# Performance work log

Hardware: AMD Instinct MI355X
Metric: run time of the kernel (lower is better)

## Reference

```python
import jax, jax.numpy as jnp
import numpy as np

N = 50000       # nodes
E = 1600000     # edges (avg degree 32)
IN = 64         # in_channels
ED = 16         # edge_dim
H = 128         # hidden_channels


def setup_inputs() -> dict:
    key = jax.random.key(0)
    ks = jax.random.split(key, 32)
    rn = lambda k, shape, s: jax.random.normal(k, shape, jnp.float32) * s
    inp = {}
    inp['x'] = rn(ks[0], (N, IN), 1.0)
    inp['edge_index'] = jax.random.randint(ks[1], (2, E), 0, N, dtype=jnp.int64)
    inp['edge_attr'] = rn(ks[2], (E, ED), 1.0)
    # per-layer params: edge linear (ED -> node_dim), MLP (d_in->H, H->H)
    node_dims = [IN, H, H]
    i = 3
    for l, d in enumerate(node_dims):
        inp[f'We{l}'] = rn(ks[i], (ED, d), 1.0 / np.sqrt(ED)); i += 1
        inp[f'be{l}'] = jnp.zeros((d,), jnp.float32)
        inp[f'W1_{l}'] = rn(ks[i], (d, H), 1.0 / np.sqrt(d)); i += 1
        inp[f'b1_{l}'] = jnp.zeros((H,), jnp.float32)
        inp[f'W2_{l}'] = rn(ks[i], (H, H), 1.0 / np.sqrt(H)); i += 1
        inp[f'b2_{l}'] = jnp.zeros((H,), jnp.float32)
    inp['Wlin'] = rn(ks[i], (H, 1), 1.0 / np.sqrt(H))
    inp['blin'] = jnp.zeros((1,), jnp.float32)
    return inp


def gine_conv(x, src, dst, ea, We, be, W1, b1, W2, b2):
    # message: relu(x_j + Lin_e(edge_attr)); aggregate: sum into dst; eps=0
    msg = jax.nn.relu(x[src] + ea @ We + be)            # [E, d]
    agg = jax.ops.segment_sum(msg, dst, num_segments=x.shape[0])  # [N, d]
    h = x + agg                                          # (1+eps)*x + agg, eps=0
    return jax.nn.relu(h @ W1 + b1) @ W2 + b2            # MLP


def reference(x, edge_index, edge_attr,
              We0, be0, W1_0, b1_0, W2_0, b2_0,
              We1, be1, W1_1, b1_1, W2_1, b2_1,
              We2, be2, W1_2, b1_2, W2_2, b2_2,
              Wlin, blin):
    src, dst = edge_index[0], edge_index[1]
    h = jax.nn.relu(gine_conv(x, src, dst, edge_attr, We0, be0, W1_0, b1_0, W2_0, b2_0))
    h = jax.nn.relu(gine_conv(h, src, dst, edge_attr, We1, be1, W1_1, b1_1, W2_1, b2_1))
    h = jax.nn.relu(gine_conv(h, src, dst, edge_attr, We2, be2, W1_2, b1_2, W2_2, b2_2))
    out = jax.nn.sigmoid(h @ Wlin + blin)                # [N, 1]
    return out.squeeze(-1)                               # [N]
```

## Files before the change

### kernel.cpp

```cpp
#include <hip/hip_runtime.h>
#include <math.h>


#define BLK 256

typedef __attribute__((ext_vector_type(2))) float f32x2;
typedef __attribute__((ext_vector_type(16))) float f32x16;

__device__ inline f32x2 pk_fma(f32x2 a, f32x2 b, f32x2 c) {
    f32x2 d;
    asm("v_pk_fma_f32 %0, %1, %2, %3" : "=v"(d) : "v"(a), "v"(b), "v"(c));
    return d;
}
__device__ inline f32x2 pk_fma_s(f32x2 a, f32x2 b, f32x2 c) {
    f32x2 d;
    asm("v_pk_fma_f32 %0, %1, %2, %3" : "=v"(d) : "s"(a), "v"(b), "v"(c));
    return d;
}
__device__ inline f32x16 sload16(const float* p) {
    f32x16 r;
    asm volatile("s_load_dwordx16 %0, %1, 0x0" : "=s"(r) : "s"(p));
    return r;
}


__global__ void detect_kernel(const unsigned int* __restrict__ ei, int* __restrict__ flag) {
    int t = blockIdx.x * blockDim.x + threadIdx.x;
    if (t < 1024) {
        if (ei[2 * t + 1] != 0u) atomicOr(flag, 1);
    }
}

__global__ void convert_hist_kernel(const int* __restrict__ ei32, const long long* __restrict__ ei64,
                                    const int* __restrict__ flag, int E,
                                    unsigned int* __restrict__ drank,
                                    int* __restrict__ counts) {
    int e = blockIdx.x * blockDim.x + threadIdx.x;
    if (e >= E) return;
    int d;
    if (*flag) d = ei32[E + e];
    else       d = (int)ei64[E + e];
    unsigned int r = (unsigned int)atomicAdd(&counts[d], 1);
    drank[e] = (unsigned int)d | (r << 16);
}

__global__ void scan_kernel(const int* __restrict__ counts, int* __restrict__ offsets, int n) {
    __shared__ int tsum[256];
    __shared__ int texcl[256];
    int t = threadIdx.x;
    int chunk = (n + 255) >> 8;
    int b = t * chunk, e = min(b + chunk, n);
    int s = 0;
    for (int i = b; i < e; i++) s += counts[i];
    tsum[t] = s;
    __syncthreads();
    if (t == 0) {
        int run = 0;
        for (int i = 0; i < 256; i++) { texcl[i] = run; run += tsum[i]; }
        offsets[n] = run;
    }
    __syncthreads();
    int run = texcl[t];
    for (int i = b; i < e; i++) { offsets[i] = run; run += counts[i]; }
}

__global__ void scatter_perm_kernel(const unsigned int* __restrict__ drank,
                                    const int* __restrict__ offsets,
                                    int* __restrict__ perm, int E) {
    int e = blockIdx.x * blockDim.x + threadIdx.x;
    if (e >= E) return;
    unsigned int v = drank[e];
    perm[offsets[v & 0xffffu] + (int)(v >> 16)] = e;
}

__global__ __launch_bounds__(256) void gather_ea_kernel(
    const int* __restrict__ perm,
    const int* __restrict__ ei32, const long long* __restrict__ ei64,
    const int* __restrict__ flag,
    const float4* __restrict__ ea4,
    int* __restrict__ srcp, float4* __restrict__ eap4, int E) {
    int t = blockIdx.x * blockDim.x + threadIdx.x;
    int p = t >> 2, q = t & 3;
    if (p >= E) return;
    int e = perm[p];
    if (q == 0) {
        int s;
        if (*flag) s = ei32[e];
        else       s = (int)ei64[e];
        srcp[p] = s;
    }
    eap4[(size_t)p * 4 + q] = ea4[(size_t)e * 4 + q];
}


__global__ __launch_bounds__(256) void aggregate64s_kernel(
    const float* __restrict__ x, const float* __restrict__ eap,
    const int* __restrict__ srcp,
    const float* __restrict__ We, const float* __restrict__ be,
    const int* __restrict__ offsets,
    float* __restrict__ h, int n) {
    constexpr int D = 64;
    int lane = threadIdx.x & 63;
    int node = __builtin_amdgcn_readfirstlane(blockIdx.x * 4 + (threadIdx.x >> 6));
    if (node >= n) return;
    int c0 = lane;

    f32x2 wp[8];
#pragma unroll
    for (int t = 0; t < 8; t++) {
        f32x2 v; v.x = We[(2 * t) * D + c0]; v.y = We[(2 * t + 1) * D + c0];
        wp[t] = v;
    }
    float bias = be[c0];
    float acc  = x[(size_t)node * D + c0];
    int p  = __builtin_amdgcn_readfirstlane(offsets[node]);
    int pe = __builtin_amdgcn_readfirstlane(offsets[node + 1]);

    for (; p + 4 <= pe; p += 4) {
        f32x16 r0 = sload16(eap + (size_t)p * 16);
        f32x16 r1 = sload16(eap + (size_t)(p + 1) * 16);
        f32x16 r2 = sload16(eap + (size_t)(p + 2) * 16);
        f32x16 r3 = sload16(eap + (size_t)(p + 3) * 16);
        int s0 = srcp[p], s1 = srcp[p + 1], s2 = srcp[p + 2], s3 = srcp[p + 3];
        float xv0 = x[(size_t)s0 * D + c0];
        float xv1 = x[(size_t)s1 * D + c0];
        float xv2 = x[(size_t)s2 * D + c0];
        float xv3 = x[(size_t)s3 * D + c0];
        asm volatile("s_waitcnt lgkmcnt(0)" : "+s"(r0), "+s"(r1), "+s"(r2), "+s"(r3));
#define EDGE_S(RU, XV)                                          \
        {                                                       \
            f32x2 prod; prod.x = (XV) + bias; prod.y = 0.f;     \
            _Pragma("unroll")                                   \
            for (int t = 0; t < 8; t++) {                       \
                f32x2 e; e.x = RU[2 * t]; e.y = RU[2 * t + 1];  \
                prod = pk_fma_s(e, wp[t], prod);                \
            }                                                   \
            acc += fmaxf(prod.x + prod.y, 0.f);                 \
        }
        EDGE_S(r0, xv0)
        EDGE_S(r1, xv1)
        EDGE_S(r2, xv2)
        EDGE_S(r3, xv3)
#undef EDGE_S
    }
    for (; p < pe; p++) {
        int s = srcp[p];
        float xv0 = x[(size_t)s * D + c0];
        const float4* er = (const float4*)(eap + (size_t)p * 16);
        float4 e0 = er[0], e1 = er[1], e2 = er[2], e3 = er[3];
        f32x2 ev[8];
        ev[0].x = e0.x; ev[0].y = e0.y;  ev[1].x = e0.z; ev[1].y = e0.w;
        ev[2].x = e1.x; ev[2].y = e1.y;  ev[3].x = e1.z; ev[3].y = e1.w;
        ev[4].x = e2.x; ev[4].y = e2.y;  ev[5].x = e2.z; ev[5].y = e2.w;
        ev[6].x = e3.x; ev[6].y = e3.y;  ev[7].x = e3.z; ev[7].y = e3.w;
        f32x2 prod; prod.x = xv0 + bias; prod.y = 0.f;
#pragma unroll
        for (int t = 0; t < 8; t++) prod = pk_fma(ev[t], wp[t], prod);
        acc += fmaxf(prod.x + prod.y, 0.f);
    }
    h[(size_t)node * D + c0] = acc;
}

__global__ __launch_bounds__(256) void aggregate128s_kernel(
    const float* __restrict__ x, const float* __restrict__ eap,
    const int* __restrict__ srcp,
    const float* __restrict__ We, const float* __restrict__ be,
    const int* __restrict__ offsets,
    float* __restrict__ h, int n) {
    constexpr int D = 128;
    int lane = threadIdx.x & 63;
    int node = __builtin_amdgcn_readfirstlane(blockIdx.x * 4 + (threadIdx.x >> 6));
    if (node >= n) return;
    int c0 = lane * 2;

    f32x2 wp[2][8];
#pragma unroll
    for (int j = 0; j < 2; j++)
#pragma unroll
        for (int t = 0; t < 8; t++) {
            f32x2 v; v.x = We[(2 * t) * D + c0 + j]; v.y = We[(2 * t + 1) * D + c0 + j];
            wp[j][t] = v;
        }
    float bias[2], acc[2];
#pragma unroll
    for (int j = 0; j < 2; j++) {
        bias[j] = be[c0 + j];
        acc[j]  = x[(size_t)node * D + c0 + j];
    }
    int p  = __builtin_amdgcn_readfirstlane(offsets[node]);
    int pe = __builtin_amdgcn_readfirstlane(offsets[node + 1]);

    for (; p + 4 <= pe; p += 4) {
        f32x16 r0 = sload16(eap + (size_t)p * 16);
        f32x16 r1 = sload16(eap + (size_t)(p + 1) * 16);
        f32x16 r2 = sload16(eap + (size_t)(p + 2) * 16);
        f32x16 r3 = sload16(eap + (size_t)(p + 3) * 16);
        int s0 = srcp[p], s1 = srcp[p + 1], s2 = srcp[p + 2], s3 = srcp[p + 3];
        float2 xv0 = *(const float2*)(x + (size_t)s0 * D + c0);
        float2 xv1 = *(const float2*)(x + (size_t)s1 * D + c0);
        float2 xv2 = *(const float2*)(x + (size_t)s2 * D + c0);
        float2 xv3 = *(const float2*)(x + (size_t)s3 * D + c0);
        asm volatile("s_waitcnt lgkmcnt(0)" : "+s"(r0), "+s"(r1), "+s"(r2), "+s"(r3));
#define EDGE_S2(RU, XV)                                             \
        {                                                           \
            f32x2 p0; p0.x = (XV).x + bias[0]; p0.y = 0.f;          \
            f32x2 p1; p1.x = (XV).y + bias[1]; p1.y = 0.f;          \
            _Pragma("unroll")                                       \
            for (int t = 0; t < 8; t++) {                           \
                f32x2 e; e.x = RU[2 * t]; e.y = RU[2 * t + 1];      \
                p0 = pk_fma_s(e, wp[0][t], p0);                     \
                p1 = pk_fma_s(e, wp[1][t], p1);                     \
            }                                                       \
            acc[0] += fmaxf(p0.x + p0.y, 0.f);                      \
            acc[1] += fmaxf(p1.x + p1.y, 0.f);                      \
        }
        EDGE_S2(r0, xv0)
        EDGE_S2(r1, xv1)
        EDGE_S2(r2, xv2)
        EDGE_S2(r3, xv3)
#undef EDGE_S2
    }
    for (; p < pe; p++) {
        int s = srcp[p];
        float2 xv = *(const float2*)(x + (size_t)s * D + c0);
        const float4* er = (const float4*)(eap + (size_t)p * 16);
        float4 e0 = er[0], e1 = er[1], e2 = er[2], e3 = er[3];
        f32x2 ev[8];
        ev[0].x = e0.x; ev[0].y = e0.y;  ev[1].x = e0.z; ev[1].y = e0.w;
        ev[2].x = e1.x; ev[2].y = e1.y;  ev[3].x = e1.z; ev[3].y = e1.w;
        ev[4].x = e2.x; ev[4].y = e2.y;  ev[5].x = e2.z; ev[5].y = e2.w;
        ev[6].x = e3.x; ev[6].y = e3.y;  ev[7].x = e3.z; ev[7].y = e3.w;
        f32x2 p0; p0.x = xv.x + bias[0]; p0.y = 0.f;
        f32x2 p1; p1.x = xv.y + bias[1]; p1.y = 0.f;
#pragma unroll
        for (int t = 0; t < 8; t++) {
            p0 = pk_fma(ev[t], wp[0][t], p0);
            p1 = pk_fma(ev[t], wp[1][t], p1);
        }
        acc[0] += fmaxf(p0.x + p0.y, 0.f);
        acc[1] += fmaxf(p1.x + p1.y, 0.f);
    }
    *(float2*)(h + (size_t)node * D + c0) = make_float2(acc[0], acc[1]);
}

template <int K>
__global__ __launch_bounds__(256) void gemm_kernel(
    const float* __restrict__ A, const float* __restrict__ B,
    const float* __restrict__ bias, float* __restrict__ C, int n) {
    __shared__ __align__(16) float As[16][36];
    __shared__ __align__(16) float Bs[16][128];
    int t = threadIdx.x;
    int row0 = blockIdx.x * 32;
    int tr = t >> 5, tc = t & 31;
    float acc[4][4];
#pragma unroll
    for (int r = 0; r < 4; r++)
#pragma unroll
        for (int c = 0; c < 4; c++) acc[r][c] = 0.f;

    int lr = t & 31, lk = (t >> 5) * 2;
    int bk = t >> 4, bc = (t & 15) * 8;

    int grow = row0 + lr;
    const float* aptr = A + (size_t)grow * K + lk;
    float2 a;
    if (grow < n) a = *(const float2*)aptr;
    else a = make_float2(0.f, 0.f);
    const float4* bp = (const float4*)(B + (size_t)bk * 128 + bc);
    float4 b0 = bp[0], b1 = bp[1];

#pragma unroll 1
    for (int ks = 0; ks < K; ks += 16) {
        As[lk + 0][lr] = a.x; As[lk + 1][lr] = a.y;
        *(float4*)&Bs[bk][bc] = b0;
        *(float4*)&Bs[bk][bc + 4] = b1;
        __syncthreads();
        if (ks + 16 < K) {
            if (grow < n) a = *(const float2*)(aptr + ks + 16);
            const float4* bp2 = (const float4*)(B + (size_t)(ks + 16 + bk) * 128 + bc);
            b0 = bp2[0]; b1 = bp2[1];
        }
#pragma unroll
        for (int kk = 0; kk < 16; kk++) {
            float4 a0 = *(const float4*)&As[kk][tr * 4];
            float4 bv = *(const float4*)&Bs[kk][tc * 4];
            float ar[4] = {a0.x, a0.y, a0.z, a0.w};
            float bc4[4] = {bv.x, bv.y, bv.z, bv.w};
#pragma unroll
            for (int r = 0; r < 4; r++)
#pragma unroll
                for (int c = 0; c < 4; c++) acc[r][c] = fmaf(ar[r], bc4[c], acc[r][c]);
        }
        __syncthreads();
    }
    float4 bb = *(const float4*)(bias + tc * 4);
#pragma unroll
    for (int r = 0; r < 4; r++) {
        int gr = row0 + tr * 4 + r;
        if (gr < n) {
            float4 v;
            v.x = fmaxf(acc[r][0] + bb.x, 0.f);
            v.y = fmaxf(acc[r][1] + bb.y, 0.f);
            v.z = fmaxf(acc[r][2] + bb.z, 0.f);
            v.w = fmaxf(acc[r][3] + bb.w, 0.f);
            *(float4*)(C + (size_t)gr * 128 + tc * 4) = v;
        }
    }
}

__global__ __launch_bounds__(256) void final_kernel(
    const float* __restrict__ x, const float* __restrict__ Wlin,
    const float* __restrict__ blin, float* __restrict__ out, int n) {
    int lane = threadIdx.x & 63;
    int node = blockIdx.x * 4 + (threadIdx.x >> 6);
    if (node >= n) return;
    float2 w = *(const float2*)(Wlin + lane * 2);
    float2 xv = *(const float2*)(x + (size_t)node * 128 + lane * 2);
    float v = xv.x * w.x + xv.y * w.y;
#pragma unroll
    for (int off = 32; off; off >>= 1) v += __shfl_down(v, off, 64);
    if (lane == 0) out[node] = 1.f / (1.f + expf(-(v + blin[0])));
}

extern "C" void kernel_launch(void* const* d_in, const int* in_sizes, int n_in,
                              void* d_out, int out_size, void* d_ws, size_t ws_size,
                              hipStream_t stream) {
    const float* x_in = (const float*)d_in[0];
    const void* ei    = d_in[1];
    const float* ea   = (const float*)d_in[2];
    const float* We[3]  = {(const float*)d_in[3], (const float*)d_in[9],  (const float*)d_in[15]};
    const float* be[3]  = {(const float*)d_in[4], (const float*)d_in[10], (const float*)d_in[16]};
    const float* W1[3]  = {(const float*)d_in[5], (const float*)d_in[11], (const float*)d_in[17]};
    const float* b1[3]  = {(const float*)d_in[6], (const float*)d_in[12], (const float*)d_in[18]};
    const float* W2[3]  = {(const float*)d_in[7], (const float*)d_in[13], (const float*)d_in[19]};
    const float* b2[3]  = {(const float*)d_in[8], (const float*)d_in[14], (const float*)d_in[20]};
    const float* Wlin = (const float*)d_in[21];
    const float* blin = (const float*)d_in[22];
    float* out = (float*)d_out;

    const int N = in_sizes[0] / 64;
    const int E = in_sizes[1] / 2;

    size_t off = 0;
    auto alloc = [&](size_t bytes) {
        void* p = (char*)d_ws + off;
        off += (bytes + 255) & ~(size_t)255;
        return p;
    };
    int*          flag    = (int*)alloc(4);
    unsigned int* drank   = (unsigned int*)alloc((size_t)E * 4);
    int*          counts  = (int*)alloc((size_t)N * 4);
    int*          offsets = (int*)alloc((size_t)(N + 1) * 4);
    int*          perm    = (int*)alloc((size_t)E * 4);
    int*          srcp    = (int*)alloc((size_t)E * 4);
    float*        eap     = (float*)alloc((size_t)E * 16 * 4);
    float*        bufA    = (float*)alloc((size_t)N * 128 * 4);
    float*        bufB    = (float*)alloc((size_t)N * 128 * 4);
    float*        bufC    = (float*)alloc((size_t)N * 128 * 4);

    hipMemsetAsync(flag, 0, 4, stream);
    hipMemsetAsync(counts, 0, (size_t)N * 4, stream);

    int egrid = (E + BLK - 1) / BLK;
    detect_kernel<<<4, BLK, 0, stream>>>((const unsigned int*)ei, flag);
    convert_hist_kernel<<<egrid, BLK, 0, stream>>>((const int*)ei, (const long long*)ei, flag, E,
                                                   drank, counts);
    scan_kernel<<<1, BLK, 0, stream>>>(counts, offsets, N);
    scatter_perm_kernel<<<egrid, BLK, 0, stream>>>(drank, offsets, perm, E);
    int g4grid = ((E * 4) + BLK - 1) / BLK;
    gather_ea_kernel<<<g4grid, BLK, 0, stream>>>(perm, (const int*)ei, (const long long*)ei, flag,
                                                 (const float4*)ea, srcp, (float4*)eap, E);

    int ngrid4 = (N + 3) / 4;
    int ggrid  = (N + 31) / 32;

    aggregate64s_kernel<<<ngrid4, BLK, 0, stream>>>(x_in, eap, srcp, We[0], be[0], offsets, bufA, N);
    gemm_kernel<64><<<ggrid, BLK, 0, stream>>>(bufA, W1[0], b1[0], bufB, N);
    gemm_kernel<128><<<ggrid, BLK, 0, stream>>>(bufB, W2[0], b2[0], bufC, N);
    aggregate128s_kernel<<<ngrid4, BLK, 0, stream>>>(bufC, eap, srcp, We[1], be[1], offsets, bufA, N);
    gemm_kernel<128><<<ggrid, BLK, 0, stream>>>(bufA, W1[1], b1[1], bufB, N);
    gemm_kernel<128><<<ggrid, BLK, 0, stream>>>(bufB, W2[1], b2[1], bufC, N);
    aggregate128s_kernel<<<ngrid4, BLK, 0, stream>>>(bufC, eap, srcp, We[2], be[2], offsets, bufA, N);
    gemm_kernel<128><<<ggrid, BLK, 0, stream>>>(bufA, W1[2], b1[2], bufB, N);
    gemm_kernel<128><<<ggrid, BLK, 0, stream>>>(bufB, W2[2], b2[2], bufC, N);

    final_kernel<<<ngrid4, BLK, 0, stream>>>(bufC, Wlin, blin, out, N);
}
```

Measured before the change: 938.5 us.

## Replace FP32 SIMT GEMMs with split-bf16 MFMA GEMMs using pre-split weights

Swaps the shared-memory FP32 FMA GEMM for a wave-level MFMA GEMM. Activations are split on the fly into bf16 hi/lo parts, and the weights are split once per call by a new conversion kernel into transposed hi/lo bf16 arrays. Each product uses three bf16 MFMAs (hi*hi, hi*lo, lo*hi) to stay close to FP32 accuracy while using the matrix cores. The cost is an extra small kernel launch, no LDS reuse of B (read from global/L2 per wave), and slightly reduced precision from dropping the lo*lo term.

Result: slower. 976.6 us (+4.1%).

```diff
diff --git a/kernel.cpp b/kernel.cpp
--- a/kernel.cpp
+++ b/kernel.cpp
@@ -6,6 +6,8 @@
 
 typedef __attribute__((ext_vector_type(2))) float f32x2;
 typedef __attribute__((ext_vector_type(16))) float f32x16;
+typedef __attribute__((ext_vector_type(8))) short bf16x8;
+typedef __attribute__((ext_vector_type(4))) float f32x4;
 
 __device__ inline f32x2 pk_fma(f32x2 a, f32x2 b, f32x2 c) {
     f32x2 d;
@@ -90,6 +92,32 @@
         srcp[p] = s;
     }
     eap4[(size_t)p * 4 + q] = ea4[(size_t)e * 4 + q];
+}
+
+struct WConvArgs {
+    const float* src[6];
+    short* hi[6];
+    short* lo[6];
+    int K[6];
+};
+
+__global__ void wconv_kernel(WConvArgs a) {
+    int b = blockIdx.x;
+    int m, base;
+    if (b < 32) { m = 0; base = 0; }
+    else { m = 1 + (b - 32) / 64; base = 32 + (m - 1) * 64; }
+    int idx = (b - base) * 256 + threadIdx.x;
+    int K = a.K[m];
+    if (idx >= K * 128) return;
+    int k = idx >> 7, nn = idx & 127;
+    float w = a.src[m][idx];
+    unsigned bits = __float_as_uint(w);
+    short hi = (short)(bits >> 16);
+    float hif = __uint_as_float(bits & 0xffff0000u);
+    float r = w - hif;
+    short lo = (short)(__float_as_uint(r) >> 16);
+    a.hi[m][(size_t)nn * K + k] = hi;
+    a.lo[m][(size_t)nn * K + k] = lo;
 }
 
 
@@ -244,66 +272,56 @@
 }
 
 template <int K>
-__global__ __launch_bounds__(256) void gemm_kernel(
-    const float* __restrict__ A, const float* __restrict__ B,
-    const float* __restrict__ bias, float* __restrict__ C, int n) {
-    __shared__ __align__(16) float As[16][36];
-    __shared__ __align__(16) float Bs[16][128];
-    int t = threadIdx.x;
-    int row0 = blockIdx.x * 32;
-    int tr = t >> 5, tc = t & 31;
-    float acc[4][4];
-#pragma unroll
-    for (int r = 0; r < 4; r++)
-#pragma unroll
-        for (int c = 0; c < 4; c++) acc[r][c] = 0.f;
-
-    int lr = t & 31, lk = (t >> 5) * 2;
-    int bk = t >> 4, bc = (t & 15) * 8;
-
-    int grow = row0 + lr;
-    const float* aptr = A + (size_t)grow * K + lk;
-    float2 a;
-    if (grow < n) a = *(const float2*)aptr;
-    else a = make_float2(0.f, 0.f);
-    const float4* bp = (const float4*)(B + (size_t)bk * 128 + bc);
-    float4 b0 = bp[0], b1 = bp[1];
+__global__ __launch_bounds__(256) void gemm_mfma_kernel(
+    const float* __restrict__ A, const short* __restrict__ Bh,
+    const short* __restrict__ Bl, const float* __restrict__ bias,
+    float* __restrict__ C, int n) {
+    int w = threadIdx.x >> 6;
+    int l = threadIdx.x & 63;
+    int row0 = blockIdx.x * 64 + w * 16;
+    if (row0 >= n) return;
+    int m  = l & 15;
+    int kg = l >> 4;
+
+    f32x4 acc[8];
+#pragma unroll
+    for (int t = 0; t < 8; t++) acc[t] = (f32x4)(0.f);
+
+    const float* arow = A + (size_t)(row0 + m) * K + kg * 8;
 
 #pragma unroll 1
-    for (int ks = 0; ks < K; ks += 16) {
-        As[lk + 0][lr] = a.x; As[lk + 1][lr] = a.y;
-        *(float4*)&Bs[bk][bc] = b0;
-        *(float4*)&Bs[bk][bc + 4] = b1;
-        __syncthreads();
-        if (ks + 16 < K) {
-            if (grow < n) a = *(const float2*)(aptr + ks + 16);
-            const float4* bp2 = (const float4*)(B + (size_t)(ks + 16 + bk) * 128 + bc);
-            b0 = bp2[0]; b1 = bp2[1];
-        }
-#pragma unroll
-        for (int kk = 0; kk < 16; kk++) {
-            float4 a0 = *(const float4*)&As[kk][tr * 4];
-            float4 bv = *(const float4*)&Bs[kk][tc * 4];
-            float ar[4] = {a0.x, a0.y, a0.z, a0.w};
-            float bc4[4] = {bv.x, bv.y, bv.z, bv.w};
-#pragma unroll
-            for (int r = 0; r < 4; r++)
-#pragma unroll
-                for (int c = 0; c < 4; c++) acc[r][c] = fmaf(ar[r], bc4[c], acc[r][c]);
-        }
-        __syncthreads();
-    }
-    float4 bb = *(const float4*)(bias + tc * 4);
-#pragma unroll
-    for (int r = 0; r < 4; r++) {
-        int gr = row0 + tr * 4 + r;
-        if (gr < n) {
-            float4 v;
-            v.x = fmaxf(acc[r][0] + bb.x, 0.f);
-            v.y = fmaxf(acc[r][1] + bb.y, 0.f);
-            v.z = fmaxf(acc[r][2] + bb.z, 0.f);
-            v.w = fmaxf(acc[r][3] + bb.w, 0.f);
-            *(float4*)(C + (size_t)gr * 128 + tc * 4) = v;
+    for (int k0 = 0; k0 < K; k0 += 32) {
+        float4 a01 = *(const float4*)(arow + k0);
+        float4 a23 = *(const float4*)(arow + k0 + 4);
+        float av[8] = {a01.x, a01.y, a01.z, a01.w, a23.x, a23.y, a23.z, a23.w};
+        bf16x8 ah, al;
+#pragma unroll
+        for (int j = 0; j < 8; j++) {
+            unsigned b = __float_as_uint(av[j]);
+            ah[j] = (short)(b >> 16);
+            float hif = __uint_as_float(b & 0xffff0000u);
+            float r = av[j] - hif;
+            al[j] = (short)(__float_as_uint(r) >> 16);
+        }
+#pragma unroll
+        for (int t = 0; t < 8; t++) {
+            const short* bp = Bh + (size_t)(t * 16 + m) * K + k0 + kg * 8;
+            const short* lp = Bl + (size_t)(t * 16 + m) * K + k0 + kg * 8;
+            bf16x8 bh = *(const bf16x8*)bp;
+            bf16x8 bl = *(const bf16x8*)lp;
+            acc[t] = __builtin_amdgcn_mfma_f32_16x16x32_bf16(ah, bh, acc[t], 0, 0, 0);
+            acc[t] = __builtin_amdgcn_mfma_f32_16x16x32_bf16(ah, bl, acc[t], 0, 0, 0);
+            acc[t] = __builtin_amdgcn_mfma_f32_16x16x32_bf16(al, bh, acc[t], 0, 0, 0);
+        }
+    }
+#pragma unroll
+    for (int t = 0; t < 8; t++) {
+        int col = t * 16 + m;
+        float bb = bias[col];
+#pragma unroll
+        for (int r = 0; r < 4; r++) {
+            int gr = row0 + kg * 4 + r;
+            C[(size_t)gr * 128 + col] = fmaxf(acc[t][r] + bb, 0.f);
         }
     }
 }
@@ -357,6 +375,13 @@
     float*        bufA    = (float*)alloc((size_t)N * 128 * 4);
     float*        bufB    = (float*)alloc((size_t)N * 128 * 4);
     float*        bufC    = (float*)alloc((size_t)N * 128 * 4);
+    short* wh[6]; short* wl[6];
+    const float* wsrc[6] = {W1[0], W2[0], W1[1], W2[1], W1[2], W2[2]};
+    int wk[6] = {64, 128, 128, 128, 128, 128};
+    for (int i = 0; i < 6; i++) {
+        wh[i] = (short*)alloc((size_t)wk[i] * 128 * 2);
+        wl[i] = (short*)alloc((size_t)wk[i] * 128 * 2);
+    }
 
     hipMemsetAsync(flag, 0, 4, stream);
     hipMemsetAsync(counts, 0, (size_t)N * 4, stream);
@@ -371,18 +396,22 @@
     gather_ea_kernel<<<g4grid, BLK, 0, stream>>>(perm, (const int*)ei, (const long long*)ei, flag,
                                                  (const float4*)ea, srcp, (float4*)eap, E);
 
+    WConvArgs wa;
+    for (int i = 0; i < 6; i++) { wa.src[i] = wsrc[i]; wa.hi[i] = wh[i]; wa.lo[i] = wl[i]; wa.K[i] = wk[i]; }
+    wconv_kernel<<<32 + 5 * 64, BLK, 0, stream>>>(wa);
+
     int ngrid4 = (N + 3) / 4;
-    int ggrid  = (N + 31) / 32;
+    int mgrid  = (N + 63) / 64;
 
     aggregate64s_kernel<<<ngrid4, BLK, 0, stream>>>(x_in, eap, srcp, We[0], be[0], offsets, bufA, N);
-    gemm_kernel<64><<<ggrid, BLK, 0, stream>>>(bufA, W1[0], b1[0], bufB, N);
-    gemm_kernel<128><<<ggrid, BLK, 0, stream>>>(bufB, W2[0], b2[0], bufC, N);
+    gemm_mfma_kernel<64><<<mgrid, BLK, 0, stream>>>(bufA, wh[0], wl[0], b1[0], bufB, N);
+    gemm_mfma_kernel<128><<<mgrid, BLK, 0, stream>>>(bufB, wh[1], wl[1], b2[0], bufC, N);
     aggregate128s_kernel<<<ngrid4, BLK, 0, stream>>>(bufC, eap, srcp, We[1], be[1], offsets, bufA, N);
-    gemm_kernel<128><<<ggrid, BLK, 0, stream>>>(bufA, W1[1], b1[1], bufB, N);
-    gemm_kernel<128><<<ggrid, BLK, 0, stream>>>(bufB, W2[1], b2[1], bufC, N);
+    gemm_mfma_kernel<128><<<mgrid, BLK, 0, stream>>>(bufA, wh[2], wl[2], b1[1], bufB, N);
+    gemm_mfma_kernel<128><<<mgrid, BLK, 0, stream>>>(bufB, wh[3], wl[3], b2[1], bufC, N);
     aggregate128s_kernel<<<ngrid4, BLK, 0, stream>>>(bufC, eap, srcp, We[2], be[2], offsets, bufA, N);
-    gemm_kernel<128><<<ggrid, BLK, 0, stream>>>(bufA, W1[2], b1[2], bufB, N);
-    gemm_kernel<128><<<ggrid, BLK, 0, stream>>>(bufB, W2[2], b2[2], bufC, N);
+    gemm_mfma_kernel<128><<<mgrid, BLK, 0, stream>>>(bufA, wh[4], wl[4], b1[2], bufB, N);
+    gemm_mfma_kernel<128><<<mgrid, BLK, 0, stream>>>(bufB, wh[5], wl[5], b2[2], bufC, N);
 
     final_kernel<<<ngrid4, BLK, 0, stream>>>(bufC, Wlin, blin, out, N);
 }
```
